# Optimization experiments

Measured on AMD Instinct MI355X. Metric: run time of the kernel, lower is better.

## Reference

```python
import jax, jax.numpy as jnp
import numpy as np

LN_EPS = 1e-5


def setup_inputs() -> dict:
    key = jax.random.key(0)
    ks = jax.random.split(key, 6)
    B, S, D = 4, 4096, 2048
    Db = D // 4  # bottleneck_dim = n_embd // compression_ratio
    hidden = jax.random.normal(ks[0], (B, S, D), dtype=jnp.float32)
    # LayerNorm params (torch defaults: gamma=1, beta=0)
    ln_gamma = jnp.ones((D,), dtype=jnp.float32)
    ln_beta = jnp.zeros((D,), dtype=jnp.float32)
    # Linear weights, torch default init: U(-1/sqrt(fan_in), 1/sqrt(fan_in))
    bd_lim = 1.0 / np.sqrt(D)
    W_down = jax.random.uniform(ks[1], (D, Db), minval=-bd_lim, maxval=bd_lim, dtype=jnp.float32)
    b_down = jax.random.uniform(ks[2], (Db,), minval=-bd_lim, maxval=bd_lim, dtype=jnp.float32)
    bu_lim = 1.0 / np.sqrt(Db)
    W_up = jax.random.uniform(ks[3], (Db, D), minval=-bu_lim, maxval=bu_lim, dtype=jnp.float32)
    b_up = jax.random.uniform(ks[4], (D,), minval=-bu_lim, maxval=bu_lim, dtype=jnp.float32)
    alpha = jnp.array(0.01, dtype=jnp.float32)
    return {
        "hidden": hidden,
        "ln_gamma": ln_gamma,
        "ln_beta": ln_beta,
        "W_down": W_down,
        "b_down": b_down,
        "W_up": W_up,
        "b_up": b_up,
        "alpha": alpha,
        "layer_idx": 0,
    }


def reference(hidden, ln_gamma, ln_beta, W_down, b_down, W_up, b_up, alpha, layer_idx):
    # LayerNorm over last dim
    mu = jnp.mean(hidden, axis=-1, keepdims=True)
    var = jnp.mean(jnp.square(hidden - mu), axis=-1, keepdims=True)
    h_norm = (hidden - mu) * jax.lax.rsqrt(var + LN_EPS) * ln_gamma + ln_beta
    # down-proj -> SiLU -> up-proj   [b s d] @ [d k] -> [b s k] -> [b s d]
    z = jnp.einsum("bsd,dk->bsk", h_norm, W_down) + b_down
    z = jax.nn.silu(z)
    bottleneck_out = jnp.einsum("bsk,kd->bsd", z, W_up) + b_up
    # alpha-gated residual
    return hidden + alpha * (bottleneck_out - hidden)
```

## Files before the change

### kernel.cpp

```cpp
#include <hip/hip_runtime.h>

typedef __bf16 bf16x8 __attribute__((ext_vector_type(8)));
typedef __bf16 bf16x4 __attribute__((ext_vector_type(4)));
typedef float f32x4 __attribute__((ext_vector_type(4)));

#define S_BARRIER() asm volatile("s_barrier" ::: "memory")
#define WAITCNT_VM(n) asm volatile("s_waitcnt vmcnt(" #n ")" ::: "memory")
#define WAITCNT_LGKM0() asm volatile("s_waitcnt lgkmcnt(0)" ::: "memory")

__global__ __launch_bounds__(256) void prep_ln_kernel(
    const float* __restrict__ Wd, __bf16* __restrict__ Wtd,
    const float* __restrict__ Wu, __bf16* __restrict__ Wtu,
    const float* __restrict__ x, const float* __restrict__ g,
    const float* __restrict__ be, __bf16* __restrict__ y,
    int D, int Db, int ntiles) {
    if ((int)blockIdx.x < ntiles) {
        const float* W;
        __bf16* Wt;
        int K, N, tile;
        const int ntile_d = (Db / 32) * (D / 32);
        if ((int)blockIdx.x < ntile_d) {
            W = Wd; Wt = Wtd; K = D; N = Db; tile = blockIdx.x;
        } else {
            W = Wu; Wt = Wtu; K = Db; N = D; tile = blockIdx.x - ntile_d;
        }
        const int tn = tile % (N / 32), tk = tile / (N / 32);
        const int n0 = tn * 32, k0 = tk * 32;
        __shared__ float t[32][33];
        const int c = threadIdx.x & 31, r0 = threadIdx.x >> 5;
#pragma unroll
        for (int r = r0; r < 32; r += 8)
            t[r][c] = W[(size_t)(k0 + r) * N + n0 + c];
        __syncthreads();
#pragma unroll
        for (int r = r0; r < 32; r += 8)
            Wt[(size_t)(n0 + r) * K + k0 + c] = (__bf16)t[c][r];
        return;
    }
    const int t = threadIdx.x;
    const size_t row = blockIdx.x - ntiles;
    const float4* xr = (const float4*)(x + row * (size_t)D);
    const int nv = D >> 3;
    float s = 0.f, ss = 0.f;
    for (int i = t; i < nv; i += 256) {
        float4 v0 = xr[i * 2], v1 = xr[i * 2 + 1];
        s += v0.x + v0.y + v0.z + v0.w + v1.x + v1.y + v1.z + v1.w;
        ss += v0.x * v0.x + v0.y * v0.y + v0.z * v0.z + v0.w * v0.w +
              v1.x * v1.x + v1.y * v1.y + v1.z * v1.z + v1.w * v1.w;
    }
    for (int o = 32; o > 0; o >>= 1) {
        s += __shfl_down(s, o);
        ss += __shfl_down(ss, o);
    }
    __shared__ float ps[4], pss[4], mv[2];
    int w = t >> 6;
    if ((t & 63) == 0) { ps[w] = s; pss[w] = ss; }
    __syncthreads();
    if (t == 0) {
        float S = ps[0] + ps[1] + ps[2] + ps[3];
        float SS = pss[0] + pss[1] + pss[2] + pss[3];
        float mu = S / (float)D;
        float var = SS / (float)D - mu * mu;
        mv[0] = mu;
        mv[1] = rsqrtf(var + 1e-5f);
    }
    __syncthreads();
    float mu = mv[0], rstd = mv[1];
    const float4* gg = (const float4*)g;
    const float4* bb = (const float4*)be;
    bf16x8* yr = (bf16x8*)(y + row * (size_t)D);
    for (int i = t; i < nv; i += 256) {
        float4 v0 = xr[i * 2], v1 = xr[i * 2 + 1];
        float4 g0 = gg[i * 2], g1 = gg[i * 2 + 1];
        float4 b0 = bb[i * 2], b1 = bb[i * 2 + 1];
        bf16x8 o;
        o[0] = (__bf16)((v0.x - mu) * rstd * g0.x + b0.x);
        o[1] = (__bf16)((v0.y - mu) * rstd * g0.y + b0.y);
        o[2] = (__bf16)((v0.z - mu) * rstd * g0.z + b0.z);
        o[3] = (__bf16)((v0.w - mu) * rstd * g0.w + b0.w);
        o[4] = (__bf16)((v1.x - mu) * rstd * g1.x + b1.x);
        o[5] = (__bf16)((v1.y - mu) * rstd * g1.y + b1.y);
        o[6] = (__bf16)((v1.z - mu) * rstd * g1.z + b1.z);
        o[7] = (__bf16)((v1.w - mu) * rstd * g1.w + b1.w);
        yr[i] = o;
    }
}

template <int EPI>
__global__ __launch_bounds__(256, 4) void gemm_bt(const __bf16* __restrict__ A,
                                                  const __bf16* __restrict__ Bt,
                                                  const float* __restrict__ bias,
                                                  const float* __restrict__ hid,
                                                  const float* __restrict__ alpha_p,
                                                  void* __restrict__ Cout,
                                                  int M, int N, int K) {
    constexpr int BM = 128, BN = 128, BK = 32;
    __shared__ __align__(16) __bf16 Ads[2][BM * BK];
    __shared__ __align__(16) __bf16 Bds[2][BN * BK];

    const int tid = threadIdx.x;
    const int wave = tid >> 6;
    const int lane = tid & 63;
    const int bn = blockIdx.x, bm = blockIdx.y;
    const int row0 = bm * BM, col0 = bn * BN;
    const int wr = wave >> 1, wc = wave & 1;

    f32x4 acc[4][4] = {};

    const __bf16* Ag = A + (size_t)row0 * K;
    const __bf16* Bg = Bt + (size_t)col0 * K;
    const int lrow = lane >> 2;
    const int lk = ((lane & 3) ^ (lrow & 3)) * 8;

    const int c = lane & 15;
    const int q = lane >> 4;

    auto stage = [&](int k0, int b) {
#pragma unroll
        for (int p = 0; p < 2; ++p) {
            const int r = wave * 32 + p * 16;
            __builtin_amdgcn_global_load_lds(
                (__attribute__((address_space(1))) void*)(Ag + (size_t)(r + lrow) * K + k0 + lk),
                (__attribute__((address_space(3))) void*)(&Ads[b][r * BK]),
                16, 0, 0);
            __builtin_amdgcn_global_load_lds(
                (__attribute__((address_space(1))) void*)(Bg + (size_t)(r + lrow) * K + k0 + lk),
                (__attribute__((address_space(3))) void*)(&Bds[b][r * BK]),
                16, 0, 0);
        }
    };

    const int nk = K / BK;
    stage(0, 0);
    for (int it = 0; it < nk; ++it) {
        const int cur = it & 1;
        if (it + 1 < nk) {
            stage((it + 1) * BK, cur ^ 1);
            WAITCNT_VM(4);
        } else {
            WAITCNT_VM(0);
        }
        S_BARRIER();

        bf16x8 afW[4], bfA[4];
#pragma unroll
        for (int j = 0; j < 4; ++j) {
            const int rl = wc * 64 + j * 16 + c;
            afW[j] = *(const bf16x8*)(&Bds[cur][rl * BK + ((q ^ (c & 3)) * 8)]);
        }
#pragma unroll
        for (int i = 0; i < 4; ++i) {
            const int rl = wr * 64 + i * 16 + c;
            bfA[i] = *(const bf16x8*)(&Ads[cur][rl * BK + ((q ^ (c & 3)) * 8)]);
        }
#pragma unroll
        for (int i = 0; i < 4; ++i)
#pragma unroll
            for (int j = 0; j < 4; ++j)
                acc[i][j] = __builtin_amdgcn_mfma_f32_16x16x32_bf16(afW[j], bfA[i],
                                                                    acc[i][j], 0, 0, 0);
        WAITCNT_LGKM0();
        S_BARRIER();
    }

    float alpha = (EPI == 1) ? *alpha_p : 0.f;
#pragma unroll
    for (int i = 0; i < 4; ++i) {
        const int rowg = row0 + wr * 64 + i * 16 + c;
#pragma unroll
        for (int j = 0; j < 4; ++j) {
            const int colb = col0 + wc * 64 + j * 16 + q * 4;
            const float4 bv = *(const float4*)(bias + colb);
            float v0 = acc[i][j][0] + bv.x;
            float v1 = acc[i][j][1] + bv.y;
            float v2 = acc[i][j][2] + bv.z;
            float v3 = acc[i][j][3] + bv.w;
            const size_t idx = (size_t)rowg * N + colb;
            if (EPI == 0) {
                bf16x4 o;
                o[0] = (__bf16)(v0 / (1.f + __expf(-v0)));
                o[1] = (__bf16)(v1 / (1.f + __expf(-v1)));
                o[2] = (__bf16)(v2 / (1.f + __expf(-v2)));
                o[3] = (__bf16)(v3 / (1.f + __expf(-v3)));
                *(bf16x4*)((__bf16*)Cout + idx) = o;
            } else {
                const float4 h = *(const float4*)(hid + idx);
                float4 o;
                o.x = h.x + alpha * (v0 - h.x);
                o.y = h.y + alpha * (v1 - h.y);
                o.z = h.z + alpha * (v2 - h.z);
                o.w = h.w + alpha * (v3 - h.w);
                *(float4*)((float*)Cout + idx) = o;
            }
        }
    }
}

extern "C" void kernel_launch(void* const* d_in, const int* in_sizes, int n_in,
                              void* d_out, int out_size, void* d_ws, size_t ws_size,
                              hipStream_t stream) {
    const float* hidden = (const float*)d_in[0];
    const float* ln_gamma = (const float*)d_in[1];
    const float* ln_beta = (const float*)d_in[2];
    const float* W_down = (const float*)d_in[3];
    const float* b_down = (const float*)d_in[4];
    const float* W_up = (const float*)d_in[5];
    const float* b_up = (const float*)d_in[6];
    const float* alpha = (const float*)d_in[7];
    float* out = (float*)d_out;

    const int D = in_sizes[2];
    const int Db = in_sizes[4];
    const int M = in_sizes[0] / D;

    char* w = (char*)d_ws;
    __bf16* hn = (__bf16*)w;  w += (size_t)M * D * sizeof(__bf16);
    __bf16* z = (__bf16*)w;   w += (size_t)M * Db * sizeof(__bf16);
    __bf16* Wtd = (__bf16*)w; w += (size_t)D * Db * sizeof(__bf16);
    __bf16* Wtu = (__bf16*)w; w += (size_t)Db * D * sizeof(__bf16);

    const int ntiles = 2 * (D / 32) * (Db / 32);
    prep_ln_kernel<<<ntiles + M, 256, 0, stream>>>(W_down, Wtd, W_up, Wtu,
                                                   hidden, ln_gamma, ln_beta, hn,
                                                   D, Db, ntiles);

    gemm_bt<0><<<dim3(Db / 128, M / 128), 256, 0, stream>>>(
        hn, Wtd, b_down, nullptr, nullptr, (void*)z, M, Db, D);

    gemm_bt<1><<<dim3(D / 128, M / 128), 256, 0, stream>>>(
        z, Wtu, b_up, hidden, alpha, (void*)out, M, D, Db);
}
```

Baseline: 394.3 us.

## Fuse LayerNorm apply into first GEMM and triple-buffer both GEMMs

The prep kernel now only computes per-row mean and rstd (one wave per row) instead of writing a normalized bf16 copy of the activations. The first GEMM reads fp32 hidden directly, applies the normalization with gamma/beta in registers, converts to bf16 and writes into LDS, so the 64 MB-scale bf16 intermediate write and read are removed. Both GEMMs move from double to triple buffering with a two-stage prefetch, and the XOR swizzle on LDS tiles is dropped. In exchange, each GEMM1 block re-reads fp32 A rows for every N-tile (4 column blocks), LDS use grows, and removing the swizzle may bring back LDS bank conflicts.

```diff
diff --git a/kernel.cpp b/kernel.cpp
--- a/kernel.cpp
+++ b/kernel.cpp
@@ -6,13 +6,13 @@
 
 #define S_BARRIER() asm volatile("s_barrier" ::: "memory")
 #define WAITCNT_VM(n) asm volatile("s_waitcnt vmcnt(" #n ")" ::: "memory")
+#define WAITCNT_VM0() asm volatile("s_waitcnt vmcnt(0)" ::: "memory")
 #define WAITCNT_LGKM0() asm volatile("s_waitcnt lgkmcnt(0)" ::: "memory")
 
-__global__ __launch_bounds__(256) void prep_ln_kernel(
+__global__ __launch_bounds__(256) void prep_stats_kernel(
     const float* __restrict__ Wd, __bf16* __restrict__ Wtd,
     const float* __restrict__ Wu, __bf16* __restrict__ Wtu,
-    const float* __restrict__ x, const float* __restrict__ g,
-    const float* __restrict__ be, __bf16* __restrict__ y,
+    const float* __restrict__ x, float2* __restrict__ stats,
     int D, int Db, int ntiles) {
     if ((int)blockIdx.x < ntiles) {
         const float* W;
@@ -37,83 +37,161 @@
             Wt[(size_t)(n0 + r) * K + k0 + c] = (__bf16)t[c][r];
         return;
     }
-    const int t = threadIdx.x;
-    const size_t row = blockIdx.x - ntiles;
+    const int wid = threadIdx.x >> 6, lane = threadIdx.x & 63;
+    const size_t row = (size_t)(blockIdx.x - ntiles) * 4 + wid;
     const float4* xr = (const float4*)(x + row * (size_t)D);
-    const int nv = D >> 3;
+    const int nv = D >> 2;
     float s = 0.f, ss = 0.f;
-    for (int i = t; i < nv; i += 256) {
-        float4 v0 = xr[i * 2], v1 = xr[i * 2 + 1];
-        s += v0.x + v0.y + v0.z + v0.w + v1.x + v1.y + v1.z + v1.w;
-        ss += v0.x * v0.x + v0.y * v0.y + v0.z * v0.z + v0.w * v0.w +
-              v1.x * v1.x + v1.y * v1.y + v1.z * v1.z + v1.w * v1.w;
+    for (int i = lane; i < nv; i += 64) {
+        float4 v = xr[i];
+        s += v.x + v.y + v.z + v.w;
+        ss += v.x * v.x + v.y * v.y + v.z * v.z + v.w * v.w;
     }
     for (int o = 32; o > 0; o >>= 1) {
         s += __shfl_down(s, o);
         ss += __shfl_down(ss, o);
     }
-    __shared__ float ps[4], pss[4], mv[2];
-    int w = t >> 6;
-    if ((t & 63) == 0) { ps[w] = s; pss[w] = ss; }
-    __syncthreads();
-    if (t == 0) {
-        float S = ps[0] + ps[1] + ps[2] + ps[3];
-        float SS = pss[0] + pss[1] + pss[2] + pss[3];
-        float mu = S / (float)D;
-        float var = SS / (float)D - mu * mu;
-        mv[0] = mu;
-        mv[1] = rsqrtf(var + 1e-5f);
-    }
-    __syncthreads();
-    float mu = mv[0], rstd = mv[1];
-    const float4* gg = (const float4*)g;
-    const float4* bb = (const float4*)be;
-    bf16x8* yr = (bf16x8*)(y + row * (size_t)D);
-    for (int i = t; i < nv; i += 256) {
-        float4 v0 = xr[i * 2], v1 = xr[i * 2 + 1];
-        float4 g0 = gg[i * 2], g1 = gg[i * 2 + 1];
-        float4 b0 = bb[i * 2], b1 = bb[i * 2 + 1];
-        bf16x8 o;
-        o[0] = (__bf16)((v0.x - mu) * rstd * g0.x + b0.x);
-        o[1] = (__bf16)((v0.y - mu) * rstd * g0.y + b0.y);
-        o[2] = (__bf16)((v0.z - mu) * rstd * g0.z + b0.z);
-        o[3] = (__bf16)((v0.w - mu) * rstd * g0.w + b0.w);
-        o[4] = (__bf16)((v1.x - mu) * rstd * g1.x + b1.x);
-        o[5] = (__bf16)((v1.y - mu) * rstd * g1.y + b1.y);
-        o[6] = (__bf16)((v1.z - mu) * rstd * g1.z + b1.z);
-        o[7] = (__bf16)((v1.w - mu) * rstd * g1.w + b1.w);
-        yr[i] = o;
-    }
-}
-
-template <int EPI>
-__global__ __launch_bounds__(256, 4) void gemm_bt(const __bf16* __restrict__ A,
-                                                  const __bf16* __restrict__ Bt,
-                                                  const float* __restrict__ bias,
-                                                  const float* __restrict__ hid,
-                                                  const float* __restrict__ alpha_p,
-                                                  void* __restrict__ Cout,
-                                                  int M, int N, int K) {
+    if (lane == 0) {
+        float mu = s / (float)D;
+        float var = ss / (float)D - mu * mu;
+        stats[row] = make_float2(mu, rsqrtf(var + 1e-5f));
+    }
+}
+
+__global__ __launch_bounds__(256) void gemm1_ln(
+    const float* __restrict__ H, const float2* __restrict__ stats,
+    const float* __restrict__ gamma, const float* __restrict__ beta,
+    const __bf16* __restrict__ Bt, const float* __restrict__ bias,
+    __bf16* __restrict__ Z, int M, int N, int K) {
     constexpr int BM = 128, BN = 128, BK = 32;
-    __shared__ __align__(16) __bf16 Ads[2][BM * BK];
-    __shared__ __align__(16) __bf16 Bds[2][BN * BK];
-
-    const int tid = threadIdx.x;
-    const int wave = tid >> 6;
-    const int lane = tid & 63;
-    const int bn = blockIdx.x, bm = blockIdx.y;
-    const int row0 = bm * BM, col0 = bn * BN;
+    __shared__ __align__(16) __bf16 Ads[3][BM * BK];
+    __shared__ __align__(16) __bf16 Bds[3][BN * BK];
+
+    const int tid = threadIdx.x, wave = tid >> 6, lane = tid & 63;
+    const int row0 = blockIdx.y * BM, col0 = blockIdx.x * BN;
     const int wr = wave >> 1, wc = wave & 1;
-
+    f32x4 acc[4][4] = {};
+
+    const __bf16* Bg = Bt + (size_t)col0 * K;
+    const int lrow = lane >> 2, lk = (lane & 3) * 8;
+
+    const int arow = tid >> 1, akoff = (tid & 1) * 16;
+    const float* Arow = H + (size_t)(row0 + arow) * K;
+    const float2 st = stats[row0 + arow];
+    const float mu = st.x, rstd = st.y;
+    float4 R[2][4], g4[4], b4[4];
+
+    auto stageB = [&](int k0, int b) {
+#pragma unroll
+        for (int p = 0; p < 2; ++p) {
+            const int r = wave * 32 + p * 16;
+            __builtin_amdgcn_global_load_lds(
+                (__attribute__((address_space(1))) void*)(Bg + (size_t)(r + lrow) * K + k0 + lk),
+                (__attribute__((address_space(3))) void*)(&Bds[b][r * BK]),
+                16, 0, 0);
+        }
+    };
+    auto loadA = [&](int k0, int rb) {
+#pragma unroll
+        for (int i = 0; i < 4; ++i)
+            R[rb][i] = *(const float4*)(Arow + k0 + akoff + i * 4);
+    };
+    auto loadGB = [&](int k0) {
+#pragma unroll
+        for (int i = 0; i < 4; ++i) {
+            g4[i] = *(const float4*)(gamma + k0 + akoff + i * 4);
+            b4[i] = *(const float4*)(beta + k0 + akoff + i * 4);
+        }
+    };
+    auto cvtWrite = [&](int rb, int b) {
+        __bf16 tmp[16];
+#pragma unroll
+        for (int i = 0; i < 4; ++i) {
+            float4 a = R[rb][i], g = g4[i], bb = b4[i];
+            tmp[i * 4 + 0] = (__bf16)((a.x - mu) * rstd * g.x + bb.x);
+            tmp[i * 4 + 1] = (__bf16)((a.y - mu) * rstd * g.y + bb.y);
+            tmp[i * 4 + 2] = (__bf16)((a.z - mu) * rstd * g.z + bb.z);
+            tmp[i * 4 + 3] = (__bf16)((a.w - mu) * rstd * g.w + bb.w);
+        }
+        *(bf16x8*)(&Ads[b][arow * BK + akoff]) = *(bf16x8*)(tmp);
+        *(bf16x8*)(&Ads[b][arow * BK + akoff + 8]) = *(bf16x8*)(tmp + 8);
+    };
+
+    const int nk = K / BK;
+    stageB(0, 0);
+    loadA(0, 0);
+    loadGB(0);
+    WAITCNT_VM0();
+    stageB(BK, 1);
+    loadA(BK, 1);
+    cvtWrite(0, 0);
+    WAITCNT_LGKM0();
+    S_BARRIER();
+
+    for (int it = 0; it < nk; ++it) {
+        const int cur = it % 3;
+        if (it + 1 < nk) loadGB((it + 1) * BK);
+        if (it + 2 < nk) {
+            stageB((it + 2) * BK, (it + 2) % 3);
+            loadA((it + 2) * BK, it & 1);
+        }
+        bf16x8 afW[4], bfA[4];
+#pragma unroll
+        for (int j = 0; j < 4; ++j)
+            afW[j] = *(const bf16x8*)(&Bds[cur][(wc * 64 + j * 16 + (lane & 15)) * BK + (lane >> 4) * 8]);
+#pragma unroll
+        for (int i = 0; i < 4; ++i)
+            bfA[i] = *(const bf16x8*)(&Ads[cur][(wr * 64 + i * 16 + (lane & 15)) * BK + (lane >> 4) * 8]);
+#pragma unroll
+        for (int i = 0; i < 4; ++i)
+#pragma unroll
+            for (int j = 0; j < 4; ++j)
+                acc[i][j] = __builtin_amdgcn_mfma_f32_16x16x32_bf16(afW[j], bfA[i],
+                                                                    acc[i][j], 0, 0, 0);
+        if (it + 1 < nk) cvtWrite((it + 1) & 1, (it + 1) % 3);
+        WAITCNT_LGKM0();
+        S_BARRIER();
+    }
+
+    const int c = lane & 15, q = lane >> 4;
+#pragma unroll
+    for (int i = 0; i < 4; ++i) {
+        const int rowg = row0 + wr * 64 + i * 16 + c;
+#pragma unroll
+        for (int j = 0; j < 4; ++j) {
+            const int colb = col0 + wc * 64 + j * 16 + q * 4;
+            const float4 bv = *(const float4*)(bias + colb);
+            float v0 = acc[i][j][0] + bv.x;
+            float v1 = acc[i][j][1] + bv.y;
+            float v2 = acc[i][j][2] + bv.z;
+            float v3 = acc[i][j][3] + bv.w;
+            bf16x4 o;
+            o[0] = (__bf16)(v0 / (1.f + __expf(-v0)));
+            o[1] = (__bf16)(v1 / (1.f + __expf(-v1)));
+            o[2] = (__bf16)(v2 / (1.f + __expf(-v2)));
+            o[3] = (__bf16)(v3 / (1.f + __expf(-v3)));
+            *(bf16x4*)(Z + (size_t)rowg * N + colb) = o;
+        }
+    }
+}
+
+__global__ __launch_bounds__(256) void gemm2_res(
+    const __bf16* __restrict__ A, const __bf16* __restrict__ Bt,
+    const float* __restrict__ bias, const float* __restrict__ hid,
+    const float* __restrict__ alpha_p, float* __restrict__ out,
+    int M, int N, int K) {
+    constexpr int BM = 128, BN = 128, BK = 32;
+    __shared__ __align__(16) __bf16 Ads[3][BM * BK];
+    __shared__ __align__(16) __bf16 Bds[3][BN * BK];
+
+    const int tid = threadIdx.x, wave = tid >> 6, lane = tid & 63;
+    const int row0 = blockIdx.y * BM, col0 = blockIdx.x * BN;
+    const int wr = wave >> 1, wc = wave & 1;
     f32x4 acc[4][4] = {};
 
     const __bf16* Ag = A + (size_t)row0 * K;
     const __bf16* Bg = Bt + (size_t)col0 * K;
-    const int lrow = lane >> 2;
-    const int lk = ((lane & 3) ^ (lrow & 3)) * 8;
-
-    const int c = lane & 15;
-    const int q = lane >> 4;
+    const int lrow = lane >> 2, lk = (lane & 3) * 8;
 
     auto stage = [&](int k0, int b) {
 #pragma unroll
@@ -132,38 +210,34 @@
 
     const int nk = K / BK;
     stage(0, 0);
+    stage(BK, 1);
+    WAITCNT_VM(4);
+    S_BARRIER();
+
     for (int it = 0; it < nk; ++it) {
-        const int cur = it & 1;
-        if (it + 1 < nk) {
-            stage((it + 1) * BK, cur ^ 1);
-            WAITCNT_VM(4);
-        } else {
-            WAITCNT_VM(0);
-        }
-        S_BARRIER();
+        const int cur = it % 3;
+        if (it + 2 < nk) stage((it + 2) * BK, (it + 2) % 3);
 
         bf16x8 afW[4], bfA[4];
 #pragma unroll
-        for (int j = 0; j < 4; ++j) {
-            const int rl = wc * 64 + j * 16 + c;
-            afW[j] = *(const bf16x8*)(&Bds[cur][rl * BK + ((q ^ (c & 3)) * 8)]);
-        }
-#pragma unroll
-        for (int i = 0; i < 4; ++i) {
-            const int rl = wr * 64 + i * 16 + c;
-            bfA[i] = *(const bf16x8*)(&Ads[cur][rl * BK + ((q ^ (c & 3)) * 8)]);
-        }
+        for (int j = 0; j < 4; ++j)
+            afW[j] = *(const bf16x8*)(&Bds[cur][(wc * 64 + j * 16 + (lane & 15)) * BK + (lane >> 4) * 8]);
+#pragma unroll
+        for (int i = 0; i < 4; ++i)
+            bfA[i] = *(const bf16x8*)(&Ads[cur][(wr * 64 + i * 16 + (lane & 15)) * BK + (lane >> 4) * 8]);
 #pragma unroll
         for (int i = 0; i < 4; ++i)
 #pragma unroll
             for (int j = 0; j < 4; ++j)
                 acc[i][j] = __builtin_amdgcn_mfma_f32_16x16x32_bf16(afW[j], bfA[i],
                                                                     acc[i][j], 0, 0, 0);
+        if (it + 2 < nk) { WAITCNT_VM(4); } else { WAITCNT_VM0(); }
         WAITCNT_LGKM0();
         S_BARRIER();
     }
 
-    float alpha = (EPI == 1) ? *alpha_p : 0.f;
+    const float alpha = *alpha_p;
+    const int c = lane & 15, q = lane >> 4;
 #pragma unroll
     for (int i = 0; i < 4; ++i) {
         const int rowg = row0 + wr * 64 + i * 16 + c;
@@ -171,27 +245,14 @@
         for (int j = 0; j < 4; ++j) {
             const int colb = col0 + wc * 64 + j * 16 + q * 4;
             const float4 bv = *(const float4*)(bias + colb);
-            float v0 = acc[i][j][0] + bv.x;
-            float v1 = acc[i][j][1] + bv.y;
-            float v2 = acc[i][j][2] + bv.z;
-            float v3 = acc[i][j][3] + bv.w;
             const size_t idx = (size_t)rowg * N + colb;
-            if (EPI == 0) {
-                bf16x4 o;
-                o[0] = (__bf16)(v0 / (1.f + __expf(-v0)));
-                o[1] = (__bf16)(v1 / (1.f + __expf(-v1)));
-                o[2] = (__bf16)(v2 / (1.f + __expf(-v2)));
-                o[3] = (__bf16)(v3 / (1.f + __expf(-v3)));
-                *(bf16x4*)((__bf16*)Cout + idx) = o;
-            } else {
-                const float4 h = *(const float4*)(hid + idx);
-                float4 o;
-                o.x = h.x + alpha * (v0 - h.x);
-                o.y = h.y + alpha * (v1 - h.y);
-                o.z = h.z + alpha * (v2 - h.z);
-                o.w = h.w + alpha * (v3 - h.w);
-                *(float4*)((float*)Cout + idx) = o;
-            }
+            const float4 h = *(const float4*)(hid + idx);
+            float4 o;
+            o.x = h.x + alpha * (acc[i][j][0] + bv.x - h.x);
+            o.y = h.y + alpha * (acc[i][j][1] + bv.y - h.y);
+            o.z = h.z + alpha * (acc[i][j][2] + bv.z - h.z);
+            o.w = h.w + alpha * (acc[i][j][3] + bv.w - h.w);
+            *(float4*)(out + idx) = o;
         }
     }
 }
@@ -214,19 +275,18 @@
     const int M = in_sizes[0] / D;
 
     char* w = (char*)d_ws;
-    __bf16* hn = (__bf16*)w;  w += (size_t)M * D * sizeof(__bf16);
-    __bf16* z = (__bf16*)w;   w += (size_t)M * Db * sizeof(__bf16);
-    __bf16* Wtd = (__bf16*)w; w += (size_t)D * Db * sizeof(__bf16);
-    __bf16* Wtu = (__bf16*)w; w += (size_t)Db * D * sizeof(__bf16);
+    __bf16* z = (__bf16*)w;     w += (size_t)M * Db * sizeof(__bf16);
+    __bf16* Wtd = (__bf16*)w;   w += (size_t)D * Db * sizeof(__bf16);
+    __bf16* Wtu = (__bf16*)w;   w += (size_t)Db * D * sizeof(__bf16);
+    float2* stats = (float2*)w; w += (size_t)M * sizeof(float2);
 
     const int ntiles = 2 * (D / 32) * (Db / 32);
-    prep_ln_kernel<<<ntiles + M, 256, 0, stream>>>(W_down, Wtd, W_up, Wtu,
-                                                   hidden, ln_gamma, ln_beta, hn,
-                                                   D, Db, ntiles);
-
-    gemm_bt<0><<<dim3(Db / 128, M / 128), 256, 0, stream>>>(
-        hn, Wtd, b_down, nullptr, nullptr, (void*)z, M, Db, D);
-
-    gemm_bt<1><<<dim3(D / 128, M / 128), 256, 0, stream>>>(
-        z, Wtu, b_up, hidden, alpha, (void*)out, M, D, Db);
-}
+    prep_stats_kernel<<<ntiles + M / 4, 256, 0, stream>>>(
+        W_down, Wtd, W_up, Wtu, hidden, stats, D, Db, ntiles);
+
+    gemm1_ln<<<dim3(Db / 128, M / 128), 256, 0, stream>>>(
+        hidden, stats, ln_gamma, ln_beta, Wtd, b_down, z, M, Db, D);
+
+    gemm2_res<<<dim3(D / 128, M / 128), 256, 0, stream>>>(
+        z, Wtu, b_up, hidden, alpha, out, M, D, Db);
+}
```

Result: slower. 556.1 us (+41.0%).
